# Kernel optimization log

Measured on AMD Instinct MI355X. Metric: run time of the kernel, lower is better.

The kernel has to match this reference:

```python
import jax, jax.numpy as jnp
import numpy as np

B, C, D, K = 2048, 1, 256, 64  # batch, channels, num variables, units per fold
NUM_LEVELS = 8                 # log2(D) levels of (product + sum)


def setup_inputs() -> dict:
    key = jax.random.key(0)
    ks = jax.random.split(key, 2 + 2 * NUM_LEVELS)
    inp = {}
    inp["x"] = jax.random.normal(ks[0], (B, C, D), dtype=jnp.float32)
    # input-layer bookkeeping: fold f reads variable f (scope of size 1)
    inp["scope_idx"] = jnp.arange(D, dtype=jnp.int32)[:, None]           # (D, 1)
    inp["w_in"] = jax.random.normal(ks[1], (D, K, C), dtype=jnp.float32) * 0.1
    F = D
    for l in range(NUM_LEVELS):
        Fo = F // 2
        # irregular fold bookkeeping: random pairing of input folds
        perm = jax.random.permutation(ks[2 + 2 * l], F)
        inp[f"idx{l}"] = perm.reshape(Fo, 2).astype(jnp.int32)           # (Fo, 2)
        inp[f"w{l}"] = (jax.random.normal(ks[3 + 2 * l], (Fo, K, K), dtype=jnp.float32)
                         * np.float32(1.0 / np.sqrt(K)))
        F = Fo
    return inp


def reference(x, scope_idx, w_in, idx0, w0, idx1, w1, idx2, w2, idx3, w3,
              idx4, w4, idx5, w5, idx6, w6, idx7, w7):
    # --- input layers: gather x[..., scope_idx] -> permute(2,1,0,3) -> (F, C, B, S=1)
    z = x[:, :, scope_idx[:, 0]]                      # (B, C, F)
    h = jnp.einsum('bcf,fkc->fbk', z, w_in)           # (F, B, K) linear input layer
    # --- inner layers: per-level gather (fold bookkeeping) + Hadamard + dense sum
    for idx, w in ((idx0, w0), (idx1, w1), (idx2, w2), (idx3, w3),
                   (idx4, w4), (idx5, w5), (idx6, w6), (idx7, w7)):
        g = h[idx]                                    # (Fo, 2, B, K) irregular gather
        p = g[:, 0] * g[:, 1]                         # Hadamard product layer
        h = jnp.einsum('fbi,foi->fbo', p, w)          # folded dense sum layer
    # --- output bookkeeping: single root fold, then transpose(0, 1)
    return jnp.transpose(h, (1, 0, 2))                # (B, 1, K)
```

## Files before the change

### kernel.cpp

```cpp
#include <hip/hip_runtime.h>


#define NTH 256

struct Params {
  const float* x;     const int* scope;  const float* w_in;
  const int* idx0; const float* w0;  const int* idx1; const float* w1;
  const int* idx2; const float* w2;  const int* idx3; const float* w3;
  const int* idx4; const float* w4;  const int* idx5; const float* w5;
  const int* idx6; const float* w6;  const int* idx7; const float* w7;
  float* beta;
  float* h1;
  float* h2;
  float* v4;
  float* out;
  int B;
};

__global__ __launch_bounds__(NTH) void k1_kernel(Params P) {
  const int t = threadIdx.x;
  if (blockIdx.x < 128) {
    const int o = blockIdx.x;
    const int a = P.idx0[2 * o], b = P.idx0[2 * o + 1];
    const int oo = t >> 2, q = t & 3;
    const float4* va4 = (const float4*)(P.w_in + (size_t)a * 64 + q * 16);
    const float4* vb4 = (const float4*)(P.w_in + (size_t)b * 64 + q * 16);
    const float4* wv4 = (const float4*)(P.w0 + (size_t)o * 4096 + oo * 64 + q * 16);
    float acc = 0.f;
    #pragma unroll
    for (int e = 0; e < 4; ++e) {
      float4 va = va4[e], vb = vb4[e], wv = wv4[e];
      acc = fmaf(va.x * vb.x, wv.x, acc);
      acc = fmaf(va.y * vb.y, wv.y, acc);
      acc = fmaf(va.z * vb.z, wv.z, acc);
      acc = fmaf(va.w * vb.w, wv.w, acc);
    }
    acc += __shfl_xor(acc, 1);
    acc += __shfl_xor(acc, 2);
    if (q == 0) P.h1[o * 64 + oo] = acc;
  } else {
    const int r = (blockIdx.x - 128) * 16 + (t >> 4);
    const int seg = t & 15;
    const float4* xp = (const float4*)(P.x + (size_t)r * 256 + seg * 16);
    float4 u0 = xp[0], u1 = xp[1], u2 = xp[2], u3 = xp[3];
    float pr = ((u0.x * u0.y) * (u0.z * u0.w)) * ((u1.x * u1.y) * (u1.z * u1.w))
             * ((u2.x * u2.y) * (u2.z * u2.w)) * ((u3.x * u3.y) * (u3.z * u3.w));
    pr *= __shfl_xor(pr, 1);
    pr *= __shfl_xor(pr, 2);
    pr *= __shfl_xor(pr, 4);
    pr *= __shfl_xor(pr, 8);
    if (seg == 0) P.beta[r] = pr;
  }
}

__global__ __launch_bounds__(NTH) void k2_kernel(Params P) {
  const int t = threadIdx.x, o = blockIdx.x;
  const int a = P.idx1[2 * o], b = P.idx1[2 * o + 1];
  const int oo = t >> 2, q = t & 3;
  const float4* va4 = (const float4*)(P.h1 + (size_t)a * 64 + q * 16);
  const float4* vb4 = (const float4*)(P.h1 + (size_t)b * 64 + q * 16);
  const float4* wv4 = (const float4*)(P.w1 + (size_t)o * 4096 + oo * 64 + q * 16);
  float acc = 0.f;
  #pragma unroll
  for (int e = 0; e < 4; ++e) {
    float4 va = va4[e], vb = vb4[e], wv = wv4[e];
    acc = fmaf(va.x * vb.x, wv.x, acc);
    acc = fmaf(va.y * vb.y, wv.y, acc);
    acc = fmaf(va.z * vb.z, wv.z, acc);
    acc = fmaf(va.w * vb.w, wv.w, acc);
  }
  acc += __shfl_xor(acc, 1);
  acc += __shfl_xor(acc, 2);
  if (q == 0) P.h2[o * 64 + oo] = acc;
}

__global__ __launch_bounds__(NTH) void k3_kernel(Params P) {
  const int t = threadIdx.x, g = blockIdx.x;
  __shared__ float v3[2][64];
  {
    const int opq = t >> 7;
    const int oo = (t >> 1) & 63, h = t & 1;
    const int aop = P.idx3[2 * g + opq];
    const int ia = P.idx2[2 * aop], ib = P.idx2[2 * aop + 1];
    const float4* va4 = (const float4*)(P.h2 + (size_t)ia * 64 + h * 32);
    const float4* vb4 = (const float4*)(P.h2 + (size_t)ib * 64 + h * 32);
    const float4* wv4 = (const float4*)(P.w2 + (size_t)aop * 4096 + oo * 64 + h * 32);
    float acc = 0.f;
    #pragma unroll
    for (int e = 0; e < 8; ++e) {
      float4 va = va4[e], vb = vb4[e], wv = wv4[e];
      acc = fmaf(va.x * vb.x, wv.x, acc);
      acc = fmaf(va.y * vb.y, wv.y, acc);
      acc = fmaf(va.z * vb.z, wv.z, acc);
      acc = fmaf(va.w * vb.w, wv.w, acc);
    }
    acc += __shfl_xor(acc, 1);
    if (h == 0) v3[opq][oo] = acc;
  }
  __syncthreads();
  {
    const int oo = t >> 2, q = t & 3;
    const float4* wv4 = (const float4*)(P.w3 + (size_t)g * 4096 + oo * 64 + q * 16);
    const float4* va4 = (const float4*)&v3[0][q * 16];
    const float4* vb4 = (const float4*)&v3[1][q * 16];
    float acc = 0.f;
    #pragma unroll
    for (int e = 0; e < 4; ++e) {
      float4 va = va4[e], vb = vb4[e], wv = wv4[e];
      acc = fmaf(va.x * vb.x, wv.x, acc);
      acc = fmaf(va.y * vb.y, wv.y, acc);
      acc = fmaf(va.z * vb.z, wv.z, acc);
      acc = fmaf(va.w * vb.w, wv.w, acc);
    }
    acc += __shfl_xor(acc, 1);
    acc += __shfl_xor(acc, 2);
    if (q == 0) P.v4[g * 64 + oo] = acc;
  }
}

__global__ __launch_bounds__(NTH) void k4_kernel(Params P) {
  const int t = threadIdx.x;
  __shared__ float VA[16][64];
  __shared__ float VB[8][64];
  __shared__ float v8[64];

  {
    const int s = t >> 4, k4 = (t & 15) * 4;
    *(float4*)&VA[s][k4] = *(const float4*)(P.v4 + s * 64 + k4);
  }
  __syncthreads();

  const float* wl[4] = {P.w4, P.w5, P.w6, P.w7};
  const int*   il[4] = {P.idx4, P.idx5, P.idx6, P.idx7};
  const int G = t >> 6, lane = t & 63;
  #pragma unroll
  for (int lev = 0; lev < 4; ++lev) {
    const int nops = 8 >> lev;
    for (int op = G; op < nops; op += 4) {
      const int i0 = il[lev][2 * op], i1 = il[lev][2 * op + 1];
      const float* a = (lev & 1) ? VB[i0] : VA[i0];
      const float* b = (lev & 1) ? VB[i1] : VA[i1];
      const float* wp = wl[lev] + (size_t)op * 4096 + lane * 64;
      float acc = 0.f;
      #pragma unroll
      for (int qq = 0; qq < 16; ++qq) {
        float4 wv = *(const float4*)(wp + 4 * qq);
        float4 av = *(const float4*)(a + 4 * qq);
        float4 bv = *(const float4*)(b + 4 * qq);
        acc = fmaf(av.x * bv.x, wv.x, acc);
        acc = fmaf(av.y * bv.y, wv.y, acc);
        acc = fmaf(av.z * bv.z, wv.z, acc);
        acc = fmaf(av.w * bv.w, wv.w, acc);
      }
      float* dst = (lev == 3) ? v8 : ((lev & 1) ? VA[op] : VB[op]);
      dst[lane] = acc;
    }
    __syncthreads();
  }

  const int r = blockIdx.x * 32 + (t >> 3);
  const int c0 = (t & 7) * 8;
  const float be = P.beta[r];
  float4 a = *(const float4*)&v8[c0];
  float4 b = *(const float4*)&v8[c0 + 4];
  float4* o4 = (float4*)(P.out + (size_t)r * 64 + c0);
  o4[0] = make_float4(be * a.x, be * a.y, be * a.z, be * a.w);
  o4[1] = make_float4(be * b.x, be * b.y, be * b.z, be * b.w);
}

extern "C" void kernel_launch(void* const* d_in, const int* in_sizes, int n_in,
                              void* d_out, int out_size, void* d_ws, size_t ws_size,
                              hipStream_t stream) {
  Params P;
  P.x     = (const float*)d_in[0];
  P.scope = (const int*)d_in[1];
  P.w_in  = (const float*)d_in[2];
  P.idx0 = (const int*)d_in[3];  P.w0 = (const float*)d_in[4];
  P.idx1 = (const int*)d_in[5];  P.w1 = (const float*)d_in[6];
  P.idx2 = (const int*)d_in[7];  P.w2 = (const float*)d_in[8];
  P.idx3 = (const int*)d_in[9];  P.w3 = (const float*)d_in[10];
  P.idx4 = (const int*)d_in[11]; P.w4 = (const float*)d_in[12];
  P.idx5 = (const int*)d_in[13]; P.w5 = (const float*)d_in[14];
  P.idx6 = (const int*)d_in[15]; P.w6 = (const float*)d_in[16];
  P.idx7 = (const int*)d_in[17]; P.w7 = (const float*)d_in[18];
  P.B    = in_sizes[0] / 256;
  float* ws = (float*)d_ws;
  P.beta = ws;
  P.h1   = ws + 2048;
  P.h2   = P.h1 + 128 * 64;
  P.v4   = P.h2 + 64 * 64;
  P.out  = (float*)d_out;

  k1_kernel<<<256, NTH, 0, stream>>>(P);
  k2_kernel<<<64,  NTH, 0, stream>>>(P);
  k3_kernel<<<16,  NTH, 0, stream>>>(P);
  k4_kernel<<<P.B / 32, NTH, 0, stream>>>(P);
}
```

Measured before the change: 26.38 us.

## Merge later stages into one persistent kernel with grid barriers and weight prefetch

Replaces the k2/k3/k4 launches with a single 256-block kernel that uses atomic-counter grid barriers between the level-1, level-2/3 and tail stages. Idle blocks prefetch w2..w7 into cache while level 1 runs. The output write is re-split to 8 rows per block. The goal is to remove launch gaps between small dependent kernels. The cost is spin-wait barriers that assume all 256 blocks are co-resident, and the sync counters depend on being reset in the prior kernel.

```diff
diff --git a/kernel.cpp b/kernel.cpp
--- a/kernel.cpp
+++ b/kernel.cpp
@@ -13,12 +13,30 @@
   float* h1;
   float* h2;
   float* v4;
+  unsigned* sync;
   float* out;
   int B;
 };
 
-__global__ __launch_bounds__(NTH) void k1_kernel(Params P) {
+__device__ inline void sinkf4(float4 v) {
+  asm volatile("" :: "v"(v.x), "v"(v.y), "v"(v.z), "v"(v.w));
+}
+
+__device__ inline void gridbar(unsigned* c, unsigned nblk) {
+  __syncthreads();
+  if (threadIdx.x == 0) {
+    __threadfence();
+    __hip_atomic_fetch_add(c, 1u, __ATOMIC_ACQ_REL, __HIP_MEMORY_SCOPE_AGENT);
+    while (__hip_atomic_load(c, __ATOMIC_ACQUIRE, __HIP_MEMORY_SCOPE_AGENT) < nblk)
+      __builtin_amdgcn_s_sleep(2);
+    __threadfence();
+  }
+  __syncthreads();
+}
+
+__global__ __launch_bounds__(NTH) void ka_kernel(Params P) {
   const int t = threadIdx.x;
+  if (blockIdx.x == 0 && t < 8) P.sync[t] = 0u;
   if (blockIdx.x < 128) {
     const int o = blockIdx.x;
     const int a = P.idx0[2 * o], b = P.idx0[2 * o + 1];
@@ -53,56 +71,26 @@
   }
 }
 
-__global__ __launch_bounds__(NTH) void k2_kernel(Params P) {
-  const int t = threadIdx.x, o = blockIdx.x;
-  const int a = P.idx1[2 * o], b = P.idx1[2 * o + 1];
-  const int oo = t >> 2, q = t & 3;
-  const float4* va4 = (const float4*)(P.h1 + (size_t)a * 64 + q * 16);
-  const float4* vb4 = (const float4*)(P.h1 + (size_t)b * 64 + q * 16);
-  const float4* wv4 = (const float4*)(P.w1 + (size_t)o * 4096 + oo * 64 + q * 16);
-  float acc = 0.f;
-  #pragma unroll
-  for (int e = 0; e < 4; ++e) {
-    float4 va = va4[e], vb = vb4[e], wv = wv4[e];
-    acc = fmaf(va.x * vb.x, wv.x, acc);
-    acc = fmaf(va.y * vb.y, wv.y, acc);
-    acc = fmaf(va.z * vb.z, wv.z, acc);
-    acc = fmaf(va.w * vb.w, wv.w, acc);
-  }
-  acc += __shfl_xor(acc, 1);
-  acc += __shfl_xor(acc, 2);
-  if (q == 0) P.h2[o * 64 + oo] = acc;
-}
-
-__global__ __launch_bounds__(NTH) void k3_kernel(Params P) {
-  const int t = threadIdx.x, g = blockIdx.x;
+__device__ inline void prefetch_seg(const float* p, int n, int slice8, int t) {
+  const int sl = n >> 3;
+  const float* base = p + slice8 * sl;
+  for (int i = t * 4; i < sl; i += NTH * 4) sinkf4(*(const float4*)(base + i));
+}
+
+__global__ __launch_bounds__(NTH) void kb_kernel(Params P) {
+  const int t = threadIdx.x, bid = blockIdx.x;
+  __shared__ float VA[16][64];
+  __shared__ float VB[8][64];
+  __shared__ float v8[64];
   __shared__ float v3[2][64];
-  {
-    const int opq = t >> 7;
-    const int oo = (t >> 1) & 63, h = t & 1;
-    const int aop = P.idx3[2 * g + opq];
-    const int ia = P.idx2[2 * aop], ib = P.idx2[2 * aop + 1];
-    const float4* va4 = (const float4*)(P.h2 + (size_t)ia * 64 + h * 32);
-    const float4* vb4 = (const float4*)(P.h2 + (size_t)ib * 64 + h * 32);
-    const float4* wv4 = (const float4*)(P.w2 + (size_t)aop * 4096 + oo * 64 + h * 32);
-    float acc = 0.f;
-    #pragma unroll
-    for (int e = 0; e < 8; ++e) {
-      float4 va = va4[e], vb = vb4[e], wv = wv4[e];
-      acc = fmaf(va.x * vb.x, wv.x, acc);
-      acc = fmaf(va.y * vb.y, wv.y, acc);
-      acc = fmaf(va.z * vb.z, wv.z, acc);
-      acc = fmaf(va.w * vb.w, wv.w, acc);
-    }
-    acc += __shfl_xor(acc, 1);
-    if (h == 0) v3[opq][oo] = acc;
-  }
-  __syncthreads();
-  {
+
+  if (bid < 64) {
+    const int o = bid;
+    const int a = P.idx1[2 * o], b = P.idx1[2 * o + 1];
     const int oo = t >> 2, q = t & 3;
-    const float4* wv4 = (const float4*)(P.w3 + (size_t)g * 4096 + oo * 64 + q * 16);
-    const float4* va4 = (const float4*)&v3[0][q * 16];
-    const float4* vb4 = (const float4*)&v3[1][q * 16];
+    const float4* va4 = (const float4*)(P.h1 + (size_t)a * 64 + q * 16);
+    const float4* vb4 = (const float4*)(P.h1 + (size_t)b * 64 + q * 16);
+    const float4* wv4 = (const float4*)(P.w1 + (size_t)o * 4096 + oo * 64 + q * 16);
     float acc = 0.f;
     #pragma unroll
     for (int e = 0; e < 4; ++e) {
@@ -114,15 +102,67 @@
     }
     acc += __shfl_xor(acc, 1);
     acc += __shfl_xor(acc, 2);
-    if (q == 0) P.v4[g * 64 + oo] = acc;
-  }
-}
-
-__global__ __launch_bounds__(NTH) void k4_kernel(Params P) {
-  const int t = threadIdx.x;
-  __shared__ float VA[16][64];
-  __shared__ float VB[8][64];
-  __shared__ float v8[64];
+    if (q == 0) P.h2[o * 64 + oo] = acc;
+  } else if (bid < 128) {
+    const int s = bid - 64;
+    #pragma unroll
+    for (int k = 0; k < 3; ++k) {
+      const int idx = s * 768 + k * 256 + t;
+      float v = (idx < 32768) ? P.w2[idx] : P.w3[idx - 32768];
+      asm volatile("" :: "v"(v));
+    }
+  } else {
+    const int p = (bid - 128) & 7;
+    prefetch_seg(P.w4, 32768, p, t);
+    prefetch_seg(P.w5, 16384, p, t);
+    prefetch_seg(P.w6, 8192, p, t);
+    prefetch_seg(P.w7, 4096, p, t);
+  }
+  gridbar(P.sync + 0, gridDim.x);
+
+  if (bid < 16) {
+    const int g = bid;
+    {
+      const int opq = t >> 7;
+      const int oo = (t >> 1) & 63, h = t & 1;
+      const int aop = P.idx3[2 * g + opq];
+      const int ia = P.idx2[2 * aop], ib = P.idx2[2 * aop + 1];
+      const float4* va4 = (const float4*)(P.h2 + (size_t)ia * 64 + h * 32);
+      const float4* vb4 = (const float4*)(P.h2 + (size_t)ib * 64 + h * 32);
+      const float4* wv4 = (const float4*)(P.w2 + (size_t)aop * 4096 + oo * 64 + h * 32);
+      float acc = 0.f;
+      #pragma unroll
+      for (int e = 0; e < 8; ++e) {
+        float4 va = va4[e], vb = vb4[e], wv = wv4[e];
+        acc = fmaf(va.x * vb.x, wv.x, acc);
+        acc = fmaf(va.y * vb.y, wv.y, acc);
+        acc = fmaf(va.z * vb.z, wv.z, acc);
+        acc = fmaf(va.w * vb.w, wv.w, acc);
+      }
+      acc += __shfl_xor(acc, 1);
+      if (h == 0) v3[opq][oo] = acc;
+    }
+    __syncthreads();
+    {
+      const int oo = t >> 2, q = t & 3;
+      const float4* wv4 = (const float4*)(P.w3 + (size_t)g * 4096 + oo * 64 + q * 16);
+      const float4* va4 = (const float4*)&v3[0][q * 16];
+      const float4* vb4 = (const float4*)&v3[1][q * 16];
+      float acc = 0.f;
+      #pragma unroll
+      for (int e = 0; e < 4; ++e) {
+        float4 va = va4[e], vb = vb4[e], wv = wv4[e];
+        acc = fmaf(va.x * vb.x, wv.x, acc);
+        acc = fmaf(va.y * vb.y, wv.y, acc);
+        acc = fmaf(va.z * vb.z, wv.z, acc);
+        acc = fmaf(va.w * vb.w, wv.w, acc);
+      }
+      acc += __shfl_xor(acc, 1);
+      acc += __shfl_xor(acc, 2);
+      if (q == 0) P.v4[g * 64 + oo] = acc;
+    }
+  }
+  gridbar(P.sync + 1, gridDim.x);
 
   {
     const int s = t >> 4, k4 = (t & 15) * 4;
@@ -158,14 +198,13 @@
     __syncthreads();
   }
 
-  const int r = blockIdx.x * 32 + (t >> 3);
-  const int c0 = (t & 7) * 8;
-  const float be = P.beta[r];
-  float4 a = *(const float4*)&v8[c0];
-  float4 b = *(const float4*)&v8[c0 + 4];
-  float4* o4 = (float4*)(P.out + (size_t)r * 64 + c0);
-  o4[0] = make_float4(be * a.x, be * a.y, be * a.z, be * a.w);
-  o4[1] = make_float4(be * b.x, be * b.y, be * b.z, be * b.w);
+  {
+    const int r = bid * 8 + (t >> 5);
+    const int c0 = (t & 31) * 2;
+    const float be = P.beta[r];
+    float2 v = *(const float2*)&v8[c0];
+    *(float2*)(P.out + (size_t)r * 64 + c0) = make_float2(be * v.x, be * v.y);
+  }
 }
 
 extern "C" void kernel_launch(void* const* d_in, const int* in_sizes, int n_in,
@@ -189,10 +228,9 @@
   P.h1   = ws + 2048;
   P.h2   = P.h1 + 128 * 64;
   P.v4   = P.h2 + 64 * 64;
+  P.sync = (unsigned*)(P.v4 + 16 * 64);
   P.out  = (float*)d_out;
 
-  k1_kernel<<<256, NTH, 0, stream>>>(P);
-  k2_kernel<<<64,  NTH, 0, stream>>>(P);
-  k3_kernel<<<16,  NTH, 0, stream>>>(P);
-  k4_kernel<<<P.B / 32, NTH, 0, stream>>>(P);
-}
+  ka_kernel<<<256, NTH, 0, stream>>>(P);
+  kb_kernel<<<256, NTH, 0, stream>>>(P);
+}
```

New measurement: 74.32 us. 182% more time.
